# Kernel tuning notes

Hardware: AMD Instinct MI355X
Metric: run time of the kernel (lower is better)

Reference implementation:

```python
import jax, jax.numpy as jnp
import numpy as np

B, L, F, DM, H, DFF, NL, PRED = 8, 1000, 7, 512, 8, 2048, 4, 50
DK = DM // H           # head dim 64
P = DK // 4            # learned-mask proj dim 16
EPS = 1e-5
SCALE = 1.0 / float(np.sqrt(DK))


def _ln(x, g, b):
    m = jnp.mean(x, -1, keepdims=True)
    v = jnp.mean((x - m) ** 2, -1, keepdims=True)
    return (x - m) / jnp.sqrt(v + EPS) * g + b


def _make_pe():
    pos = np.arange(L, dtype=np.float32)[:, None]
    div = np.exp(np.arange(0, DM, 2, dtype=np.float32) * (-np.log(10000.0) / DM))
    pe = np.zeros((L, DM), dtype=np.float32)
    pe[:, 0::2] = np.sin(pos * div)
    pe[:, 1::2] = np.cos(pos * div)
    return jnp.asarray(pe)


def setup_inputs() -> dict:
    key = jax.random.key(0)
    ks = iter(jax.random.split(key, 40))
    def w(shape, s=0.02):
        return jax.random.normal(next(ks), shape, jnp.float32) * s
    return {
        "x": jax.random.normal(next(ks), (B, L, F), jnp.float32),
        "emb_w": w((F, DM)), "emb_b": jnp.zeros((DM,), jnp.float32),
        "pe": _make_pe(),
        "Wq": w((NL, DM, DM)), "bq": jnp.zeros((NL, DM), jnp.float32),
        "Wk": w((NL, DM, DM)), "bk": jnp.zeros((NL, DM), jnp.float32),
        "Wv": w((NL, DM, DM)), "bv": jnp.zeros((NL, DM), jnp.float32),
        "Wo": w((NL, DM, DM)), "bo": jnp.zeros((NL, DM), jnp.float32),
        "W1": w((NL, DM, DFF)), "b1": jnp.zeros((NL, DFF), jnp.float32),
        "W2": w((NL, DFF, DM)), "b2": jnp.zeros((NL, DM), jnp.float32),
        "g1": jnp.ones((NL, DM), jnp.float32), "be1": jnp.zeros((NL, DM), jnp.float32),
        "g2": jnp.ones((NL, DM), jnp.float32), "be2": jnp.zeros((NL, DM), jnp.float32),
        "lm_qw": w((DK, P)), "lm_qb": jnp.zeros((P,), jnp.float32),
        "lm_kw": w((DK, P)), "lm_kb": jnp.zeros((P,), jnp.float32),
        "gn": jnp.ones((DM,), jnp.float32), "bn": jnp.zeros((DM,), jnp.float32),
        "fc_w": w((DM, PRED)), "fc_b": jnp.zeros((PRED,), jnp.float32),
    }


def reference(x, emb_w, emb_b, pe, Wq, bq, Wk, bk, Wv, bv, Wo, bo,
              W1, b1, W2, b2, g1, be1, g2, be2,
              lm_qw, lm_qb, lm_kw, lm_kb, gn, bn, fc_w, fc_b):
    # eval mode: dropout = identity
    h = x @ emb_w + emb_b + pe[None]                 # [B,L,DM]
    for i in range(NL):
        q = (h @ Wq[i] + bq[i]).reshape(B, L, H, DK)
        k = (h @ Wk[i] + bk[i]).reshape(B, L, H, DK)
        v = (h @ Wv[i] + bv[i]).reshape(B, L, H, DK)
        scores = jnp.einsum('blhd,bshd->bhls', q, k) * SCALE
        # shared LearnedMask: per-head Q/K projection to P dims, tanh bias
        qp = q @ lm_qw + lm_qb                       # [B,L,H,P]
        kp = k @ lm_kw + lm_kb                       # [B,S,H,P]
        scores = scores + jnp.tanh(jnp.einsum('blhp,bshp->bhls', qp, kp))
        attn = jax.nn.softmax(scores, axis=-1)       # mask_flag=False: no mask
        ctx = jnp.einsum('bhls,bshd->blhd', attn, v).reshape(B, L, DM)
        h = _ln(h + ctx @ Wo[i] + bo[i], g1[i], be1[i])
        y = jax.nn.relu(h @ W1[i] + b1[i]) @ W2[i] + b2[i]
        h2 = _ln(h + y, g2[i], be2[i])
        h = _ln(h2 + y, g2[i], be2[i])               # module applies norm2 twice
    h = _ln(h, gn, bn)                               # Encoder final norm
    return h[:, -1, :] @ fc_w + fc_b                 # [B, PRED]
```

## Files before the change

### kernel.cpp

```cpp
#include <hip/hip_runtime.h>
#include <math.h>

#define B_    8
#define L_    1000
#define F_    7
#define DM_   512
#define H_    8
#define DFF_  2048
#define NL_   4
#define PRED_ 50
#define DK_   64
#define P_    16
#define EPS_  1e-5f
#define QKVS  1792

#define L2E_   1.4426950408889634f
#define C_QS   0.18033688011112042f
#define BS_QP  2.8853900817779268f
#define SHFT_  24.0f

typedef unsigned short u16;
typedef __bf16 bf16x8 __attribute__((ext_vector_type(8)));
typedef float  f32x4  __attribute__((ext_vector_type(4)));

__device__ inline float wave_reduce_sum(float x) {
#pragma unroll
  for (int off = 32; off >= 1; off >>= 1) x += __shfl_xor(x, off, 64);
  return x;
}
__device__ inline u16 f2bf(float f) {
  unsigned int u = __float_as_uint(f);
  unsigned int r = u + 0x7FFFu + ((u >> 16) & 1u);
  return (u16)(r >> 16);
}
__device__ inline float bf2f(u16 u) { return __uint_as_float(((unsigned int)u) << 16); }
__device__ inline float fexp2(float x) { return __builtin_amdgcn_exp2f(x); }
__device__ inline float frcp(float x) { return __builtin_amdgcn_rcpf(x); }

union bfrag { bf16x8 b; uint4 q; u16 u[8]; };

__device__ inline void gload16(const u16* g, u16* l) {
  __builtin_amdgcn_global_load_lds(
      (const __attribute__((address_space(1))) void*)g,
      (__attribute__((address_space(3))) void*)l, 16, 0, 0);
}

__global__ __launch_bounds__(256)
void transpose_w(const float* __restrict__ in, u16* __restrict__ out,
                 int K, int N, size_t in_lstride, size_t out_lstride,
                 int row_off, int out_ld) {
  __shared__ float tile[32][33];
  int z = blockIdx.z;
  int kk0 = blockIdx.y * 32, nn0 = blockIdx.x * 32;
  int tx = threadIdx.x & 31, ty = threadIdx.x >> 5;
  const float* ip = in + z * in_lstride;
  u16* op = out + z * out_lstride;
#pragma unroll
  for (int i = 0; i < 4; i++)
    tile[ty + i * 8][tx] = ip[(size_t)(kk0 + ty + i * 8) * N + nn0 + tx];
  __syncthreads();
#pragma unroll
  for (int i = 0; i < 4; i++)
    op[(size_t)(row_off + nn0 + ty + i * 8) * out_ld + kk0 + tx] = f2bf(tile[tx][ty + i * 8]);
}

__global__ __launch_bounds__(256)
void wfuse_kernel(const float* __restrict__ Wq, const float* __restrict__ Wk,
                  const float* __restrict__ lmqw, const float* __restrict__ lmkw,
                  u16* __restrict__ Wt) {
  int hh = blockIdx.x, side = blockIdx.y, layer = blockIdx.z;
  const float* W = (side ? Wk : Wq) + (size_t)layer * 512 * 512;
  const float* lw = side ? lmkw : lmqw;
  float scale = side ? 1.0f : BS_QP;
  __shared__ float lws[64][17];
  int t = threadIdx.x;
  for (int i = t; i < 1024; i += 256) lws[i >> 4][i & 15] = lw[i];
  __syncthreads();
  int p = t & 15, kk = t >> 4;
  u16* orow = Wt + (size_t)layer * QKVS * 512 + (size_t)(1536 + side * 128 + hh * 16 + p) * 512;
  for (int kb = 0; kb < 32; kb++) {
    int k = kb * 16 + kk;
    const float* wr = W + (size_t)k * 512 + hh * 64;
    float acc = 0.f;
#pragma unroll
    for (int d = 0; d < 64; d++) acc = fmaf(wr[d], lws[d][p], acc);
    orow[k] = f2bf(acc * scale);
  }
}

__global__ __launch_bounds__(192)
void vzero_kernel(u16* __restrict__ vtg) {
  int bh = blockIdx.x;
  int t = threadIdx.x;
  int dk = t / 3, c = t - dk * 3;
  *(uint4*)(vtg + ((size_t)bh * 64 + dk) * 1024 + 1000 + c * 8) =
      make_uint4(0u, 0u, 0u, 0u);
}

__global__ __launch_bounds__(256)
void concat_bias(const float* __restrict__ bq, const float* __restrict__ bk,
                 const float* __restrict__ bv,
                 const float* __restrict__ lmqw, const float* __restrict__ lmqb,
                 const float* __restrict__ lmkw, const float* __restrict__ lmkb,
                 float* __restrict__ bqkv) {
  int i = blockIdx.x * 256 + threadIdx.x;
  int l = i / QKVS, j = i % QKVS;
  float v;
  if (j < 512) v = bq[l * 512 + j];
  else if (j < 1024) v = bk[l * 512 + j - 512];
  else if (j < 1536) v = bv[l * 512 + j - 1024];
  else if (j < 1664) {
    int hh = (j - 1536) >> 4, p = (j - 1536) & 15;
    float acc = lmqb[p];
#pragma unroll
    for (int d = 0; d < 64; d++) acc = fmaf(bq[l * 512 + hh * 64 + d], lmqw[d * 16 + p], acc);
    v = acc * BS_QP;
  } else {
    int hh = (j - 1664) >> 4, p = (j - 1664) & 15;
    float acc = lmkb[p];
#pragma unroll
    for (int d = 0; d < 64; d++) acc = fmaf(bk[l * 512 + hh * 64 + d], lmkw[d * 16 + p], acc);
    v = acc;
  }
  bqkv[i] = v;
}

__global__ __launch_bounds__(512)
void embed_kernel(const float* __restrict__ x, const float* __restrict__ emb_w,
                  const float* __restrict__ emb_b, const float* __restrict__ pe,
                  float* __restrict__ h, u16* __restrict__ h16) {
  int bl = blockIdx.x;
  int l = bl % L_;
  int d = threadIdx.x;
  const float* xr = x + (size_t)bl * F_;
  float acc = emb_b[d] + pe[(size_t)l * DM_ + d];
#pragma unroll
  for (int f = 0; f < F_; f++) acc = fmaf(xr[f], emb_w[f * DM_ + d], acc);
  h[(size_t)bl * DM_ + d] = acc;
  h16[(size_t)bl * DM_ + d] = f2bf(acc);
}

template<int BN>
__global__ __launch_bounds__(256)
void gemm16(const u16* __restrict__ A, const u16* __restrict__ Bt,
            const float* __restrict__ bias, const float* __restrict__ resid,
            float* __restrict__ C32, u16* __restrict__ C16, u16* __restrict__ vtg,
            int M, int K, int N, int relu, int nscale, float sval) {
  constexpr int NTW = BN / 32;
  constexpr int BG  = BN / 32;
  __shared__ u16 As[128 * 64];
  __shared__ u16 Bs[BN * 64];
  int t = threadIdx.x;
  int w = t >> 6, lane = t & 63;
  int wr = w >> 1, wc = w & 1;
  int mloc = lane & 15, quad = lane >> 4;
  int m0 = blockIdx.y * 128, n0 = blockIdx.x * BN;

  const u16* agp[4]; u16* alds[4];
#pragma unroll
  for (int j = 0; j < 4; j++) {
    int r = w * 32 + j * 8 + (lane >> 3);
    int gm = m0 + r; if (gm > M - 1) gm = M - 1;
    int ch = (lane & 7) ^ (r & 7);
    agp[j] = A + (size_t)gm * K + ch * 8;
    alds[j] = As + (w * 32 + j * 8) * 64;
  }
  const u16* bgp[BG]; u16* blds[BG];
#pragma unroll
  for (int j = 0; j < BG; j++) {
    int r = w * (8 * BG) + j * 8 + (lane >> 3);
    int ch = (lane & 7) ^ (r & 7);
    bgp[j] = Bt + (size_t)(n0 + r) * K + ch * 8;
    blds[j] = Bs + (w * (8 * BG) + j * 8) * 64;
  }
  const u16* apt[2][4];
#pragma unroll
  for (int mi = 0; mi < 4; mi++) {
    int tr = wr * 64 + mi * 16 + mloc;
    apt[0][mi] = As + tr * 64 + ((quad ^ (tr & 7)) * 8);
    apt[1][mi] = As + tr * 64 + (((4 + quad) ^ (tr & 7)) * 8);
  }
  const u16* bpt[2][NTW];
#pragma unroll
  for (int nt = 0; nt < NTW; nt++) {
    int tr = wc * (BN / 2) + nt * 16 + mloc;
    bpt[0][nt] = Bs + tr * 64 + ((quad ^ (tr & 7)) * 8);
    bpt[1][nt] = Bs + tr * 64 + (((4 + quad) ^ (tr & 7)) * 8);
  }

  f32x4 acc[4][NTW];
#pragma unroll
  for (int mi = 0; mi < 4; mi++)
#pragma unroll
    for (int nt = 0; nt < NTW; nt++) acc[mi][nt] = (f32x4){0.f, 0.f, 0.f, 0.f};

  for (int k0 = 0; k0 < K; k0 += 64) {
    __syncthreads();
#pragma unroll
    for (int j = 0; j < 4; j++) gload16(agp[j] + k0, alds[j]);
#pragma unroll
    for (int j = 0; j < BG; j++) gload16(bgp[j] + k0, blds[j]);
    __syncthreads();
#pragma unroll
    for (int kc = 0; kc < 2; kc++) {
      bf16x8 af[4], bv[NTW];
#pragma unroll
      for (int mi = 0; mi < 4; mi++) af[mi] = *(const bf16x8*)apt[kc][mi];
#pragma unroll
      for (int nt = 0; nt < NTW; nt++) bv[nt] = *(const bf16x8*)bpt[kc][nt];
#pragma unroll
      for (int mi = 0; mi < 4; mi++)
#pragma unroll
        for (int nt = 0; nt < NTW; nt++)
          acc[mi][nt] = __builtin_amdgcn_mfma_f32_16x16x32_bf16(af[mi], bv[nt], acc[mi][nt], 0, 0, 0);
    }
  }

#pragma unroll
  for (int mi = 0; mi < 4; mi++) {
    int m_r0 = m0 + wr * 64 + mi * 16 + quad * 4;
#pragma unroll
    for (int nt = 0; nt < NTW; nt++) {
      int nbase = n0 + wc * (BN / 2) + nt * 16;
      int n = nbase + mloc;
      if (vtg && nbase >= 1024 && nbase < 1536) {
        if (m_r0 < M) {
          int bb = (m_r0 * 67109) >> 26;
          int ll = m_r0 - bb * 1000;
          int hh2 = (n - 1024) >> 6, dk = n & 63;
          float bn_ = bias[n];
          union { uint2 d; u16 s[4]; } pk;
#pragma unroll
          for (int r = 0; r < 4; r++) pk.s[r] = f2bf(acc[mi][nt][r] + bn_);
          u16* dst = vtg + ((size_t)(bb * 8 + hh2) * 64 + dk) * 1024 + ll;
          *(uint2*)dst = pk.d;
        }
      } else {
        float bn_ = bias[n];
#pragma unroll
        for (int r = 0; r < 4; r++) {
          int m = m_r0 + r;
          if (m >= M) continue;
          size_t crow = (size_t)m * N;
          float vsum = acc[mi][nt][r] + bn_;
          if (resid) vsum += resid[crow + n];
          if (n < nscale) vsum *= sval;
          if (relu) vsum = fmaxf(vsum, 0.f);
          if (C32) C32[crow + n] = vsum;
          if (C16) C16[crow + n] = f2bf(vsum);
        }
      }
    }
  }
}

#define KT   128
#define KPLD 24
#define PSLD 40
__global__ __launch_bounds__(256)
void attn_mfma_kernel(const u16* __restrict__ qkv, const u16* __restrict__ vtg,
                      u16* __restrict__ ctx) {
  __shared__ u16 Ks[KT * 64];
  __shared__ u16 Vt[64 * KT];
  __shared__ u16 Kp[KT * KPLD];
  __shared__ u16 Ps[4 * 16 * PSLD];

  int Lid = blockIdx.x;
  int qt = Lid >> 6;
  int bh = ((Lid & 7) << 3) | ((Lid >> 3) & 7);
  int b = bh >> 3, hh = bh & 7;
  int l0 = qt * 64;
  int t = threadIdx.x;
  int wv = t >> 6, lane = t & 63;
  int m = lane & 15, quad = lane >> 4;

  int lq = l0 + wv * 16 + m; if (lq > L_ - 1) lq = L_ - 1;
  const u16* qrow = qkv + (size_t)(b * L_ + lq) * QKVS + hh * DK_;
  bf16x8 qa0 = *(const bf16x8*)(qrow + quad * 8);
  bf16x8 qa1 = *(const bf16x8*)(qrow + 32 + quad * 8);
  bfrag qpa;
  if (quad < 2) {
    qpa.q = *(const uint4*)(qkv + (size_t)(b * L_ + lq) * QKVS + 1536 + hh * P_ + quad * 8);
  } else {
    qpa.q = make_uint4(0u, 0u, 0u, 0u);
  }

  const u16* ks_g = qkv + ((size_t)b * L_ + (t >> 3)) * QKVS + 512 + hh * DK_
                    + ((t & 7) ^ ((t >> 3) & 7)) * 8;
  u16* ks_l = Ks + (t >> 6) * 512;
  const u16* vt_g = vtg + ((size_t)bh * DK_ + (t >> 4)) * 1024
                    + (((t & 15) ^ (t >> 4)) * 8);
  u16* vt_l = Vt + (t >> 6) * 512;

  f32x4 O[4];
#pragma unroll
  for (int nt = 0; nt < 4; nt++) O[nt] = (f32x4){0.f, 0.f, 0.f, 0.f};
  float lrun[4] = {0.f, 0.f, 0.f, 0.f};

  u16* pw = Ps + wv * (16 * PSLD);
  const u16* pr0 = pw + m * PSLD + quad * 8;
  const f32x4 zz = (f32x4){0.f, 0.f, 0.f, 0.f};

  for (int s0 = 0; s0 < L_; s0 += KT) {
    uint4 p0, p1;
    if (t < KT) {
      int sg2 = s0 + t; if (sg2 > L_ - 1) sg2 = L_ - 1;
      const u16* pr = qkv + (size_t)(b * L_ + sg2) * QKVS + 1664 + hh * P_;
      p0 = *(const uint4*)(pr);
      p1 = *(const uint4*)(pr + 8);
    }
    __syncthreads();
#pragma unroll
    for (int j = 0; j < 4; j++) {
      gload16(ks_g + ((size_t)s0 + j * 32) * QKVS, ks_l + j * 2048);
      gload16(vt_g + s0 + (size_t)j * 16 * 1024, vt_l + j * 2048);
    }
    if (t < KT) {
      *(uint4*)&Kp[t * KPLD]     = p0;
      *(uint4*)&Kp[t * KPLD + 8] = p1;
    }
    __syncthreads();

#pragma unroll
    for (int kc = 0; kc < 4; kc++) {
      float pv2[2][4];
#pragma unroll
      for (int h2 = 0; h2 < 2; h2++) {
        int nt = kc * 2 + h2;
        const u16* kb = Ks + (nt * 16 + m) * 64;
        int x0 = ((quad) ^ (m & 7)) * 8;
        int x1 = ((4 + quad) ^ (m & 7)) * 8;
        f32x4 sacc = __builtin_amdgcn_mfma_f32_16x16x32_bf16(qa0, *(const bf16x8*)(kb + x0), zz, 0, 0, 0);
        sacc = __builtin_amdgcn_mfma_f32_16x16x32_bf16(qa1, *(const bf16x8*)(kb + x1), sacc, 0, 0, 0);
        bf16x8 kpf = *(const bf16x8*)(Kp + (nt * 16 + m) * KPLD + (quad & 1) * 8);
        f32x4 macc = __builtin_amdgcn_mfma_f32_16x16x32_bf16(qpa.b, kpf, zz, 0, 0, 0);
        bool oob = (s0 + nt * 16 + m) >= L_;
#pragma unroll
        for (int r = 0; r < 4; r++) {
          float e = fexp2(macc[r]);
          float d = frcp(e + 1.f);
          float th = fmaf(d, -2.f * L2E_, L2E_);
          float s = sacc[r] + th;
          if (oob) s = -3e38f;
          float p = fexp2(s - SHFT_);
          pv2[h2][r] = p;
          lrun[r] += p;
        }
      }
#pragma unroll
      for (int h2 = 0; h2 < 2; h2++)
#pragma unroll
        for (int r = 0; r < 4; r++)
          pw[(quad * 4 + r) * PSLD + h2 * 16 + m] = f2bf(pv2[h2][r]);
      bf16x8 pa = *(const bf16x8*)pr0;
#pragma unroll
      for (int ntd = 0; ntd < 4; ntd++) {
        const u16* vb = Vt + (ntd * 16 + m) * KT + (((kc * 4 + quad) ^ m) * 8);
        O[ntd] = __builtin_amdgcn_mfma_f32_16x16x32_bf16(pa, *(const bf16x8*)vb, O[ntd], 0, 0, 0);
      }
    }
  }

  float inv[4];
#pragma unroll
  for (int r = 0; r < 4; r++) {
#pragma unroll
    for (int msk = 1; msk < 16; msk <<= 1) lrun[r] += __shfl_xor(lrun[r], msk, 64);
    inv[r] = frcp(lrun[r]);
  }
#pragma unroll
  for (int r = 0; r < 4; r++) {
    int l = l0 + wv * 16 + quad * 4 + r;
    if (l >= L_) continue;
    u16* crow = ctx + ((size_t)(b * L_ + l)) * DM_ + hh * DK_;
#pragma unroll
    for (int nt = 0; nt < 4; nt++) crow[nt * 16 + m] = f2bf(O[nt][r] * inv[r]);
  }
}

__global__ __launch_bounds__(256)
void ln_kernel(const float* __restrict__ a, const float* __restrict__ badd,
               const float* __restrict__ g, const float* __restrict__ be,
               float* __restrict__ o, u16* __restrict__ o16) {
  int row = blockIdx.x;
  int t = threadIdx.x;
  size_t base = (size_t)row * DM_;
  float x0 = a[base + t], x1 = a[base + t + 256];
  if (badd) { x0 += badd[base + t]; x1 += badd[base + t + 256]; }
  float s = wave_reduce_sum(x0 + x1);
  float ss = wave_reduce_sum(x0 * x0 + x1 * x1);
  __shared__ float sh_s[4], sh_ss[4];
  int wv = t >> 6, lane = t & 63;
  if (lane == 0) { sh_s[wv] = s; sh_ss[wv] = ss; }
  __syncthreads();
  float S = sh_s[0] + sh_s[1] + sh_s[2] + sh_s[3];
  float SS = sh_ss[0] + sh_ss[1] + sh_ss[2] + sh_ss[3];
  float mean = S * (1.0f / DM_);
  float var = SS * (1.0f / DM_) - mean * mean;
  float rstd = rsqrtf(var + EPS_);
  float r0 = (x0 - mean) * rstd * g[t] + be[t];
  float r1 = (x1 - mean) * rstd * g[t + 256] + be[t + 256];
  o[base + t] = r0; o[base + t + 256] = r1;
  if (o16) { o16[base + t] = f2bf(r0); o16[base + t + 256] = f2bf(r1); }
}

__global__ __launch_bounds__(256)
void ln2x_kernel(const float* __restrict__ hin, const float* __restrict__ y,
                 const float* __restrict__ g, const float* __restrict__ be,
                 float* __restrict__ o32, u16* __restrict__ o16) {
  int row = blockIdx.x;
  int t = threadIdx.x;
  size_t base = (size_t)row * DM_;
  float y0 = y[base + t], y1 = y[base + t + 256];
  float x0 = hin[base + t] + y0, x1 = hin[base + t + 256] + y1;
  __shared__ float sh_s[4], sh_ss[4];
  int wv = t >> 6, lane = t & 63;
  float g0 = g[t], g1v = g[t + 256], b0 = be[t], b1v = be[t + 256];

  float s = wave_reduce_sum(x0 + x1);
  float ss = wave_reduce_sum(x0 * x0 + x1 * x1);
  if (lane == 0) { sh_s[wv] = s; sh_ss[wv] = ss; }
  __syncthreads();
  float S = sh_s[0] + sh_s[1] + sh_s[2] + sh_s[3];
  float SS = sh_ss[0] + sh_ss[1] + sh_ss[2] + sh_ss[3];
  float mean = S * (1.0f / DM_);
  float var = SS * (1.0f / DM_) - mean * mean;
  float rstd = rsqrtf(var + EPS_);
  float h20 = (x0 - mean) * rstd * g0 + b0 + y0;
  float h21 = (x1 - mean) * rstd * g1v + b1v + y1;
  __syncthreads();

  s = wave_reduce_sum(h20 + h21);
  ss = wave_reduce_sum(h20 * h20 + h21 * h21);
  if (lane == 0) { sh_s[wv] = s; sh_ss[wv] = ss; }
  __syncthreads();
  S = sh_s[0] + sh_s[1] + sh_s[2] + sh_s[3];
  SS = sh_ss[0] + sh_ss[1] + sh_ss[2] + sh_ss[3];
  mean = S * (1.0f / DM_);
  var = SS * (1.0f / DM_) - mean * mean;
  rstd = rsqrtf(var + EPS_);
  float r0 = (h20 - mean) * rstd * g0 + b0;
  float r1 = (h21 - mean) * rstd * g1v + b1v;
  o32[base + t] = r0; o32[base + t + 256] = r1;
  if (o16) { o16[base + t] = f2bf(r0); o16[base + t + 256] = f2bf(r1); }
}

__global__ __launch_bounds__(512)
void final_kernel(const float* __restrict__ h, const float* __restrict__ gn,
                  const float* __restrict__ bn, const float* __restrict__ fcw,
                  const float* __restrict__ fcb, float* __restrict__ out) {
  int b = blockIdx.x;
  int t = threadIdx.x;
  size_t base = ((size_t)b * L_ + (L_ - 1)) * DM_;
  float x = h[base + t];
  float s = wave_reduce_sum(x);
  float ss = wave_reduce_sum(x * x);
  __shared__ float sh_s[8], sh_ss[8];
  int wv = t >> 6, lane = t & 63;
  if (lane == 0) { sh_s[wv] = s; sh_ss[wv] = ss; }
  __syncthreads();
  float S = 0.f, SS = 0.f;
#pragma unroll
  for (int i = 0; i < 8; i++) { S += sh_s[i]; SS += sh_ss[i]; }
  float mean = S * (1.0f / DM_);
  float var = SS * (1.0f / DM_) - mean * mean;
  float rstd = rsqrtf(var + EPS_);
  __shared__ float hn[DM_];
  hn[t] = (x - mean) * rstd * gn[t] + bn[t];
  __syncthreads();
  if (t < PRED_) {
    float acc = fcb[t];
#pragma unroll 8
    for (int d = 0; d < DM_; d++) acc = fmaf(hn[d], fcw[d * PRED_ + t], acc);
    out[b * PRED_ + t] = acc;
  }
}

extern "C" void kernel_launch(void* const* d_in, const int* in_sizes, int n_in,
                              void* d_out, int out_size, void* d_ws, size_t ws_size,
                              hipStream_t stream) {
  const float* x     = (const float*)d_in[0];
  const float* emb_w = (const float*)d_in[1];
  const float* emb_b = (const float*)d_in[2];
  const float* pe    = (const float*)d_in[3];
  const float* Wq = (const float*)d_in[4];  const float* bq = (const float*)d_in[5];
  const float* Wk = (const float*)d_in[6];  const float* bk = (const float*)d_in[7];
  const float* Wv = (const float*)d_in[8];  const float* bv = (const float*)d_in[9];
  const float* Wo = (const float*)d_in[10]; const float* bo = (const float*)d_in[11];
  const float* W1 = (const float*)d_in[12]; const float* b1 = (const float*)d_in[13];
  const float* W2 = (const float*)d_in[14]; const float* b2 = (const float*)d_in[15];
  const float* g1 = (const float*)d_in[16]; const float* be1 = (const float*)d_in[17];
  const float* g2 = (const float*)d_in[18]; const float* be2 = (const float*)d_in[19];
  const float* lm_qw = (const float*)d_in[20]; const float* lm_qb = (const float*)d_in[21];
  const float* lm_kw = (const float*)d_in[22]; const float* lm_kb = (const float*)d_in[23];
  const float* gn = (const float*)d_in[24]; const float* bn = (const float*)d_in[25];
  const float* fc_w = (const float*)d_in[26]; const float* fc_b = (const float*)d_in[27];
  float* out = (float*)d_out;

  const size_t ROWS = (size_t)B_ * L_;
  u16* qkv16 = (u16*)d_ws;
  u16* ctx16 = qkv16 + ROWS * QKVS;
  u16* ffn1  = qkv16;
  u16* h16   = ctx16 + ROWS * DM_;
  u16* Wqkv_t = h16 + ROWS * DM_;
  u16* Wo_t   = Wqkv_t + (size_t)NL_ * QKVS * DM_;
  u16* W1_t   = Wo_t + (size_t)NL_ * DM_ * DM_;
  u16* W2_t   = W1_t + (size_t)NL_ * DFF_ * DM_;
  float* h32  = (float*)(W2_t + (size_t)NL_ * DM_ * DFF_);
  float* t0   = h32 + ROWS * DM_;
  float* bqkv = t0 + ROWS * DM_;
  u16* vtg    = (u16*)t0;

  transpose_w<<<dim3(16, 16, NL_), 256, 0, stream>>>(Wq, Wqkv_t, DM_, DM_, (size_t)DM_ * DM_, (size_t)QKVS * DM_, 0, DM_);
  transpose_w<<<dim3(16, 16, NL_), 256, 0, stream>>>(Wk, Wqkv_t, DM_, DM_, (size_t)DM_ * DM_, (size_t)QKVS * DM_, 512, DM_);
  transpose_w<<<dim3(16, 16, NL_), 256, 0, stream>>>(Wv, Wqkv_t, DM_, DM_, (size_t)DM_ * DM_, (size_t)QKVS * DM_, 1024, DM_);
  transpose_w<<<dim3(16, 16, NL_), 256, 0, stream>>>(Wo, Wo_t, DM_, DM_, (size_t)DM_ * DM_, (size_t)DM_ * DM_, 0, DM_);
  transpose_w<<<dim3(64, 16, NL_), 256, 0, stream>>>(W1, W1_t, DM_, DFF_, (size_t)DM_ * DFF_, (size_t)DFF_ * DM_, 0, DM_);
  transpose_w<<<dim3(16, 64, NL_), 256, 0, stream>>>(W2, W2_t, DFF_, DM_, (size_t)DFF_ * DM_, (size_t)DM_ * DFF_, 0, DFF_);
  wfuse_kernel<<<dim3(H_, 2, NL_), 256, 0, stream>>>(Wq, Wk, lm_qw, lm_kw, Wqkv_t);
  concat_bias<<<NL_ * QKVS / 256, 256, 0, stream>>>(bq, bk, bv, lm_qw, lm_qb, lm_kw, lm_kb, bqkv);

  embed_kernel<<<dim3((unsigned)ROWS), 512, 0, stream>>>(x, emb_w, emb_b, pe, h32, h16);

  dim3 g_qkv(QKVS / 128, 63);
  dim3 g_ffn1(DFF_ / 128, 63);
  dim3 g_n512(DM_ / 64, 63);
  dim3 g_attn(1024);

  for (int i = 0; i < NL_; i++) {
    gemm16<128><<<g_qkv, 256, 0, stream>>>(h16, Wqkv_t + (size_t)i * QKVS * DM_,
        bqkv + i * QKVS, nullptr, nullptr, qkv16, vtg, 8000, DM_, QKVS, 0, 512, C_QS);

    vzero_kernel<<<64, 192, 0, stream>>>(vtg);

    attn_mfma_kernel<<<g_attn, 256, 0, stream>>>(qkv16, vtg, ctx16);

    gemm16<64><<<g_n512, 256, 0, stream>>>(ctx16, Wo_t + (size_t)i * DM_ * DM_,
        bo + i * DM_, h32, t0, nullptr, nullptr, 8000, DM_, DM_, 0, 0, 1.0f);
    ln_kernel<<<dim3((unsigned)ROWS), 256, 0, stream>>>(t0, nullptr, g1 + i * DM_, be1 + i * DM_, h32, h16);

    gemm16<128><<<g_ffn1, 256, 0, stream>>>(h16, W1_t + (size_t)i * DFF_ * DM_,
        b1 + i * DFF_, nullptr, nullptr, ffn1, nullptr, 8000, DM_, DFF_, 1, 0, 1.0f);
    gemm16<64><<<g_n512, 256, 0, stream>>>(ffn1, W2_t + (size_t)i * DM_ * DFF_,
        b2 + i * DM_, nullptr, t0, nullptr, nullptr, 8000, DFF_, DM_, 0, 0, 1.0f);

    ln2x_kernel<<<dim3((unsigned)ROWS), 256, 0, stream>>>(h32, t0, g2 + i * DM_, be2 + i * DM_, h32, h16);
  }

  final_kernel<<<B_, 512, 0, stream>>>(h32, gn, bn, fc_w, fc_b, out);
}
```

Baseline: 1.223 ms.

## Keep residual stream in bf16 only and shrink attention key tile

Removes the fp32 copy of the hidden state and the fp32 GEMM outputs. Residual adds, layernorms and the final norm now read and write bf16 with packed two-element accesses, which cuts global memory traffic in the epilogues and norm kernels. The attention key/value tile drops from 128 to 64 with a matching swizzle change. V-transpose storage moves to its own buffer, so the per-layer zero-padding kernel is dropped. The cost is lower numerical precision in the residual path across four layers.

```diff
diff --git a/kernel.cpp b/kernel.cpp
--- a/kernel.cpp
+++ b/kernel.cpp
@@ -33,6 +33,9 @@
   unsigned int r = u + 0x7FFFu + ((u >> 16) & 1u);
   return (u16)(r >> 16);
 }
+__device__ inline unsigned int pack2(float a, float b) {
+  return (unsigned int)f2bf(a) | ((unsigned int)f2bf(b) << 16);
+}
 __device__ inline float bf2f(u16 u) { return __uint_as_float(((unsigned int)u) << 16); }
 __device__ inline float fexp2(float x) { return __builtin_amdgcn_exp2f(x); }
 __device__ inline float frcp(float x) { return __builtin_amdgcn_rcpf(x); }
@@ -86,15 +89,6 @@
     for (int d = 0; d < 64; d++) acc = fmaf(wr[d], lws[d][p], acc);
     orow[k] = f2bf(acc * scale);
   }
-}
-
-__global__ __launch_bounds__(192)
-void vzero_kernel(u16* __restrict__ vtg) {
-  int bh = blockIdx.x;
-  int t = threadIdx.x;
-  int dk = t / 3, c = t - dk * 3;
-  *(uint4*)(vtg + ((size_t)bh * 64 + dk) * 1024 + 1000 + c * 8) =
-      make_uint4(0u, 0u, 0u, 0u);
 }
 
 __global__ __launch_bounds__(256)
@@ -128,7 +122,7 @@
 __global__ __launch_bounds__(512)
 void embed_kernel(const float* __restrict__ x, const float* __restrict__ emb_w,
                   const float* __restrict__ emb_b, const float* __restrict__ pe,
-                  float* __restrict__ h, u16* __restrict__ h16) {
+                  u16* __restrict__ h16) {
   int bl = blockIdx.x;
   int l = bl % L_;
   int d = threadIdx.x;
@@ -136,15 +130,14 @@
   float acc = emb_b[d] + pe[(size_t)l * DM_ + d];
 #pragma unroll
   for (int f = 0; f < F_; f++) acc = fmaf(xr[f], emb_w[f * DM_ + d], acc);
-  h[(size_t)bl * DM_ + d] = acc;
   h16[(size_t)bl * DM_ + d] = f2bf(acc);
 }
 
 template<int BN>
 __global__ __launch_bounds__(256)
 void gemm16(const u16* __restrict__ A, const u16* __restrict__ Bt,
-            const float* __restrict__ bias, const float* __restrict__ resid,
-            float* __restrict__ C32, u16* __restrict__ C16, u16* __restrict__ vtg,
+            const float* __restrict__ bias, const u16* __restrict__ resid,
+            u16* __restrict__ C16, u16* __restrict__ vtg,
             int M, int K, int N, int relu, int nscale, float sval) {
   constexpr int NTW = BN / 32;
   constexpr int BG  = BN / 32;
@@ -243,18 +236,17 @@
           if (m >= M) continue;
           size_t crow = (size_t)m * N;
           float vsum = acc[mi][nt][r] + bn_;
-          if (resid) vsum += resid[crow + n];
+          if (resid) vsum += bf2f(resid[crow + n]);
           if (n < nscale) vsum *= sval;
           if (relu) vsum = fmaxf(vsum, 0.f);
-          if (C32) C32[crow + n] = vsum;
-          if (C16) C16[crow + n] = f2bf(vsum);
+          C16[crow + n] = f2bf(vsum);
         }
       }
     }
   }
 }
 
-#define KT   128
+#define KT   64
 #define KPLD 24
 #define PSLD 40
 __global__ __launch_bounds__(256)
@@ -288,8 +280,8 @@
   const u16* ks_g = qkv + ((size_t)b * L_ + (t >> 3)) * QKVS + 512 + hh * DK_
                     + ((t & 7) ^ ((t >> 3) & 7)) * 8;
   u16* ks_l = Ks + (t >> 6) * 512;
-  const u16* vt_g = vtg + ((size_t)bh * DK_ + (t >> 4)) * 1024
-                    + (((t & 15) ^ (t >> 4)) * 8);
+  const u16* vt_g = vtg + ((size_t)bh * DK_ + (t >> 3)) * 1024
+                    + ((t & 7) ^ ((t >> 3) & 7)) * 8;
   u16* vt_l = Vt + (t >> 6) * 512;
 
   f32x4 O[4];
@@ -311,9 +303,9 @@
     }
     __syncthreads();
 #pragma unroll
-    for (int j = 0; j < 4; j++) {
+    for (int j = 0; j < 2; j++) {
       gload16(ks_g + ((size_t)s0 + j * 32) * QKVS, ks_l + j * 2048);
-      gload16(vt_g + s0 + (size_t)j * 16 * 1024, vt_l + j * 2048);
+      gload16(vt_g + s0 + (size_t)j * 32 * 1024, vt_l + j * 2048);
     }
     if (t < KT) {
       *(uint4*)&Kp[t * KPLD]     = p0;
@@ -322,7 +314,7 @@
     __syncthreads();
 
 #pragma unroll
-    for (int kc = 0; kc < 4; kc++) {
+    for (int kc = 0; kc < 2; kc++) {
       float pv2[2][4];
 #pragma unroll
       for (int h2 = 0; h2 < 2; h2++) {
@@ -355,7 +347,7 @@
       bf16x8 pa = *(const bf16x8*)pr0;
 #pragma unroll
       for (int ntd = 0; ntd < 4; ntd++) {
-        const u16* vb = Vt + (ntd * 16 + m) * KT + (((kc * 4 + quad) ^ m) * 8);
+        const u16* vb = Vt + (ntd * 16 + m) * KT + (((kc * 4 + quad) ^ (m & 7)) * 8);
         O[ntd] = __builtin_amdgcn_mfma_f32_16x16x32_bf16(pa, *(const bf16x8*)vb, O[ntd], 0, 0, 0);
       }
     }
@@ -379,14 +371,13 @@
 }
 
 __global__ __launch_bounds__(256)
-void ln_kernel(const float* __restrict__ a, const float* __restrict__ badd,
-               const float* __restrict__ g, const float* __restrict__ be,
-               float* __restrict__ o, u16* __restrict__ o16) {
+void ln_kernel(const u16* __restrict__ a, const float* __restrict__ g,
+               const float* __restrict__ be, u16* __restrict__ o) {
   int row = blockIdx.x;
   int t = threadIdx.x;
   size_t base = (size_t)row * DM_;
-  float x0 = a[base + t], x1 = a[base + t + 256];
-  if (badd) { x0 += badd[base + t]; x1 += badd[base + t + 256]; }
+  unsigned int av = *(const unsigned int*)(a + base + 2 * t);
+  float x0 = bf2f((u16)av), x1 = bf2f((u16)(av >> 16));
   float s = wave_reduce_sum(x0 + x1);
   float ss = wave_reduce_sum(x0 * x0 + x1 * x1);
   __shared__ float sh_s[4], sh_ss[4];
@@ -398,24 +389,25 @@
   float mean = S * (1.0f / DM_);
   float var = SS * (1.0f / DM_) - mean * mean;
   float rstd = rsqrtf(var + EPS_);
-  float r0 = (x0 - mean) * rstd * g[t] + be[t];
-  float r1 = (x1 - mean) * rstd * g[t + 256] + be[t + 256];
-  o[base + t] = r0; o[base + t + 256] = r1;
-  if (o16) { o16[base + t] = f2bf(r0); o16[base + t + 256] = f2bf(r1); }
-}
-
-__global__ __launch_bounds__(256)
-void ln2x_kernel(const float* __restrict__ hin, const float* __restrict__ y,
+  float r0 = (x0 - mean) * rstd * g[2 * t] + be[2 * t];
+  float r1 = (x1 - mean) * rstd * g[2 * t + 1] + be[2 * t + 1];
+  *(unsigned int*)(o + base + 2 * t) = pack2(r0, r1);
+}
+
+__global__ __launch_bounds__(256)
+void ln2x_kernel(const u16* __restrict__ hin, const u16* __restrict__ y,
                  const float* __restrict__ g, const float* __restrict__ be,
-                 float* __restrict__ o32, u16* __restrict__ o16) {
+                 u16* __restrict__ o16) {
   int row = blockIdx.x;
   int t = threadIdx.x;
   size_t base = (size_t)row * DM_;
-  float y0 = y[base + t], y1 = y[base + t + 256];
-  float x0 = hin[base + t] + y0, x1 = hin[base + t + 256] + y1;
+  unsigned int hv = *(const unsigned int*)(hin + base + 2 * t);
+  unsigned int yv = *(const unsigned int*)(y + base + 2 * t);
+  float y0 = bf2f((u16)yv), y1 = bf2f((u16)(yv >> 16));
+  float x0 = bf2f((u16)hv) + y0, x1 = bf2f((u16)(hv >> 16)) + y1;
   __shared__ float sh_s[4], sh_ss[4];
   int wv = t >> 6, lane = t & 63;
-  float g0 = g[t], g1v = g[t + 256], b0 = be[t], b1v = be[t + 256];
+  float g0 = g[2 * t], g1v = g[2 * t + 1], b0 = be[2 * t], b1v = be[2 * t + 1];
 
   float s = wave_reduce_sum(x0 + x1);
   float ss = wave_reduce_sum(x0 * x0 + x1 * x1);
@@ -441,18 +433,17 @@
   rstd = rsqrtf(var + EPS_);
   float r0 = (h20 - mean) * rstd * g0 + b0;
   float r1 = (h21 - mean) * rstd * g1v + b1v;
-  o32[base + t] = r0; o32[base + t + 256] = r1;
-  if (o16) { o16[base + t] = f2bf(r0); o16[base + t + 256] = f2bf(r1); }
+  *(unsigned int*)(o16 + base + 2 * t) = pack2(r0, r1);
 }
 
 __global__ __launch_bounds__(512)
-void final_kernel(const float* __restrict__ h, const float* __restrict__ gn,
+void final_kernel(const u16* __restrict__ h, const float* __restrict__ gn,
                   const float* __restrict__ bn, const float* __restrict__ fcw,
                   const float* __restrict__ fcb, float* __restrict__ out) {
   int b = blockIdx.x;
   int t = threadIdx.x;
   size_t base = ((size_t)b * L_ + (L_ - 1)) * DM_;
-  float x = h[base + t];
+  float x = bf2f(h[base + t]);
   float s = wave_reduce_sum(x);
   float ss = wave_reduce_sum(x * x);
   __shared__ float sh_s[8], sh_ss[8];
@@ -502,14 +493,13 @@
   u16* ctx16 = qkv16 + ROWS * QKVS;
   u16* ffn1  = qkv16;
   u16* h16   = ctx16 + ROWS * DM_;
-  u16* Wqkv_t = h16 + ROWS * DM_;
+  u16* t16   = h16 + ROWS * DM_;
+  u16* vtg   = t16 + ROWS * DM_;
+  u16* Wqkv_t = vtg + (size_t)64 * 64 * 1024;
   u16* Wo_t   = Wqkv_t + (size_t)NL_ * QKVS * DM_;
   u16* W1_t   = Wo_t + (size_t)NL_ * DM_ * DM_;
   u16* W2_t   = W1_t + (size_t)NL_ * DFF_ * DM_;
-  float* h32  = (float*)(W2_t + (size_t)NL_ * DM_ * DFF_);
-  float* t0   = h32 + ROWS * DM_;
-  float* bqkv = t0 + ROWS * DM_;
-  u16* vtg    = (u16*)t0;
+  float* bqkv = (float*)(W2_t + (size_t)NL_ * DM_ * DFF_);
 
   transpose_w<<<dim3(16, 16, NL_), 256, 0, stream>>>(Wq, Wqkv_t, DM_, DM_, (size_t)DM_ * DM_, (size_t)QKVS * DM_, 0, DM_);
   transpose_w<<<dim3(16, 16, NL_), 256, 0, stream>>>(Wk, Wqkv_t, DM_, DM_, (size_t)DM_ * DM_, (size_t)QKVS * DM_, 512, DM_);
@@ -520,7 +510,7 @@
   wfuse_kernel<<<dim3(H_, 2, NL_), 256, 0, stream>>>(Wq, Wk, lm_qw, lm_kw, Wqkv_t);
   concat_bias<<<NL_ * QKVS / 256, 256, 0, stream>>>(bq, bk, bv, lm_qw, lm_qb, lm_kw, lm_kb, bqkv);
 
-  embed_kernel<<<dim3((unsigned)ROWS), 512, 0, stream>>>(x, emb_w, emb_b, pe, h32, h16);
+  embed_kernel<<<dim3((unsigned)ROWS), 512, 0, stream>>>(x, emb_w, emb_b, pe, h16);
 
   dim3 g_qkv(QKVS / 128, 63);
   dim3 g_ffn1(DFF_ / 128, 63);
@@ -529,23 +519,21 @@
 
   for (int i = 0; i < NL_; i++) {
     gemm16<128><<<g_qkv, 256, 0, stream>>>(h16, Wqkv_t + (size_t)i * QKVS * DM_,
-        bqkv + i * QKVS, nullptr, nullptr, qkv16, vtg, 8000, DM_, QKVS, 0, 512, C_QS);
-
-    vzero_kernel<<<64, 192, 0, stream>>>(vtg);
+        bqkv + i * QKVS, nullptr, qkv16, vtg, 8000, DM_, QKVS, 0, 512, C_QS);
 
     attn_mfma_kernel<<<g_attn, 256, 0, stream>>>(qkv16, vtg, ctx16);
 
     gemm16<64><<<g_n512, 256, 0, stream>>>(ctx16, Wo_t + (size_t)i * DM_ * DM_,
-        bo + i * DM_, h32, t0, nullptr, nullptr, 8000, DM_, DM_, 0, 0, 1.0f);
-    ln_kernel<<<dim3((unsigned)ROWS), 256, 0, stream>>>(t0, nullptr, g1 + i * DM_, be1 + i * DM_, h32, h16);
+        bo + i * DM_, h16, t16, nullptr, 8000, DM_, DM_, 0, 0, 1.0f);
+    ln_kernel<<<dim3((unsigned)ROWS), 256, 0, stream>>>(t16, g1 + i * DM_, be1 + i * DM_, h16);
 
     gemm16<128><<<g_ffn1, 256, 0, stream>>>(h16, W1_t + (size_t)i * DFF_ * DM_,
-        b1 + i * DFF_, nullptr, nullptr, ffn1, nullptr, 8000, DM_, DFF_, 1, 0, 1.0f);
+        b1 + i * DFF_, nullptr, ffn1, nullptr, 8000, DM_, DFF_, 1, 0, 1.0f);
     gemm16<64><<<g_n512, 256, 0, stream>>>(ffn1, W2_t + (size_t)i * DM_ * DFF_,
-        b2 + i * DM_, nullptr, t0, nullptr, nullptr, 8000, DFF_, DM_, 0, 0, 1.0f);
-
-    ln2x_kernel<<<dim3((unsigned)ROWS), 256, 0, stream>>>(h32, t0, g2 + i * DM_, be2 + i * DM_, h32, h16);
-  }
-
-  final_kernel<<<B_, 512, 0, stream>>>(h32, gn, bn, fc_w, fc_b, out);
-}
+        b2 + i * DM_, nullptr, t16, nullptr, 8000, DFF_, DM_, 0, 0, 1.0f);
+
+    ln2x_kernel<<<dim3((unsigned)ROWS), 256, 0, stream>>>(h16, t16, g2 + i * DM_, be2 + i * DM_, h16);
+  }
+
+  final_kernel<<<B_, 512, 0, stream>>>(h16, gn, bn, fc_w, fc_b, out);
+}
```

Result: faster. 1.107 ms (-9.5%).
